# Optimization experiments

Hardware: AMD Instinct MI355X
Metric: run time of the kernel (lower is better)

## Reference

```python
import jax, jax.numpy as jnp
import numpy as np

H, SK, SV, PK, PV = 12, 16, 16, 4, 8
SCALAR_DIM, PAIR_DIM = 384, 128
SIZES = [SK*H, SK*H, SV*H, PK*H*3, PK*H*3, PV*H*3]  # qkv split sizes
N_LOGITS = 3
SS = (N_LOGITS * SK) ** -0.5                 # scalar logit scale
PS = (N_LOGITS * PK * 4.5) ** -0.5           # point logit scale
PBS = N_LOGITS ** -0.5                       # pair bias scale
EPS = 1e-8


def setup_inputs() -> dict:
    key = jax.random.key(0)
    ks = jax.random.split(key, 16)
    b, n = 1, 768
    scalar_feats = jax.random.normal(ks[0], (b, n, SCALAR_DIM), jnp.float32)
    pair_feats = jax.random.normal(ks[1], (b, n, n, PAIR_DIM), jnp.float32)
    rotations = jax.random.normal(ks[2], (b, n, 3, 3), jnp.float32)
    translations = jax.random.normal(ks[3], (b, n, 3), jnp.float32)
    mask = jnp.ones((b, n), dtype=bool)
    d_qkv = sum(SIZES)
    sc = SCALAR_DIM ** -0.5
    Wqkv = jax.random.normal(ks[4], (SCALAR_DIM, d_qkv), jnp.float32) * sc
    Wpb = jax.random.normal(ks[5], (PAIR_DIM, H), jnp.float32) * PAIR_DIM ** -0.5
    point_weights = jnp.full((1, H, 1, 1), float(np.log(np.e - 1.0)), jnp.float32)
    dim_out = H * (PAIR_DIM + SV + 4 * PV)  # 2112
    Wout = jax.random.normal(ks[6], (dim_out, SCALAR_DIM), jnp.float32) * dim_out ** -0.5
    bout = jnp.zeros((SCALAR_DIM,), jnp.float32)
    Wp1 = jax.random.normal(ks[7], (3 * H, PAIR_DIM), jnp.float32) * (3 * H) ** -0.5
    bp1 = jnp.zeros((PAIR_DIM,), jnp.float32)
    Wp2 = jax.random.normal(ks[8], (PAIR_DIM, PAIR_DIM), jnp.float32) * PAIR_DIM ** -0.5
    bp2 = jnp.zeros((PAIR_DIM,), jnp.float32)
    return dict(scalar_feats=scalar_feats, pair_feats=pair_feats, rotations=rotations,
                translations=translations, mask=mask, Wqkv=Wqkv, Wpb=Wpb,
                point_weights=point_weights, Wout=Wout, bout=bout,
                Wp1=Wp1, bp1=bp1, Wp2=Wp2, bp2=bp2)


def _heads(x, b, n, d):
    # b n (h d) -> b h n d
    return x.reshape(b, n, H, d).transpose(0, 2, 1, 3)


def _merge(x):
    # b h n d -> b n (h d)
    b, h, n, d = x.shape
    return x.transpose(0, 2, 1, 3).reshape(b, n, h * d)


def ipa_forward(scalar_feats, pair_feats, rotations, translations, mask,
                Wqkv, Wpb, point_weights, Wout, bout, Wp1, bp1, Wp2, bp2):
    b, n, _ = scalar_feats.shape
    qkv = scalar_feats @ Wqkv
    offs = np.cumsum([0] + SIZES)
    qs, ks_, vs, qp, kp, vp = [qkv[..., offs[i]:offs[i + 1]] for i in range(6)]
    qs, ks_, vs = _heads(qs, b, n, SK), _heads(ks_, b, n, SK), _heads(vs, b, n, SV)

    def to_global_points(p, d):
        p = p.reshape(b, n, H * d, 3)                       # ... (d c) -> ... d c
        p = jnp.einsum('bixy,bidy->bidx', rotations, p) + translations[:, :, None, :]
        return p.reshape(b, n, H, d, 3).transpose(0, 2, 1, 3, 4)  # b h n d 3

    qp, kp = to_global_points(qp, PK), to_global_points(kp, PK)
    vp = to_global_points(vp, PV)

    scalar_logits = jnp.einsum('bhid,bhjd->bhij', qs, ks_)
    pair_bias = jnp.einsum('bijd,dh->bhij', pair_feats, Wpb)
    point_logits = jnp.einsum('bhidc,bhjdc->bhij', qp, kp) * jax.nn.softplus(point_weights)

    m2 = mask[:, None, :, None] & mask[:, None, None, :]    # b 1 i j
    neg = -jnp.finfo(scalar_logits.dtype).max
    scalar_logits = jnp.where(m2, scalar_logits, neg)
    point_logits = jnp.where(m2, point_logits, neg)
    pair_bias = jnp.where(m2, pair_bias, neg)

    attn = jax.nn.softmax(SS * scalar_logits + PS * point_logits + PBS * pair_bias, axis=-1)

    res_scalar = jnp.einsum('bhij,bhjd->bhid', attn, vs)
    res_pair = jnp.einsum('bhij,bijd->bhid', attn, pair_feats)
    res_pts = jnp.einsum('bhij,bhjdc->bhidc', attn, vp)
    # inverse rigid: R^T (p - t)
    local = jnp.einsum('biyx,bhidy->bhidx', rotations,
                       res_pts - translations[:, None, :, None, :])
    pts_norm = jnp.sqrt(jnp.sum(local ** 2, axis=-1) + EPS)  # safe_norm

    feats = jnp.concatenate([
        _merge(res_scalar),                                   # b n h*SV
        _merge(res_pair),                                     # b n h*PAIR_DIM
        _merge(local.reshape(b, H, n, PV * 3)),               # b n h*PV*3
        _merge(pts_norm),                                     # b n h*PV
    ], axis=-1)
    scalar_out = feats @ Wout + bout

    edge = jnp.concatenate([attn,
                            jax.nn.softmax(point_logits, axis=-1),
                            jax.nn.softmax(scalar_logits, axis=-1)], axis=1)
    edge = edge.transpose(0, 2, 3, 1)                         # b i j (3h)
    pair_out = jax.nn.gelu(edge @ Wp1 + bp1, approximate=False) @ Wp2 + bp2
    return scalar_out, pair_out


def reference(scalar_feats, pair_feats, rotations, translations, mask,
              Wqkv, Wpb, point_weights, Wout, bout, Wp1, bp1, Wp2, bp2):
    return ipa_forward(scalar_feats, pair_feats, rotations, translations, mask,
                       Wqkv, Wpb, point_weights, Wout, bout, Wp1, bp1, Wp2, bp2)
```

## Files before the change

### kernel.cpp

```cpp
#include <hip/hip_runtime.h>
#include <hip/hip_bf16.h>
#include <math.h>

#define NRES 768
#define NH 12
#define DQKV 1152
#define PAIRD 128
#define SCD 384
#define DOUTF 2112

#define SS_C 0.14433756729740643f
#define PS_C 0.13608276348795434f
#define PBS_C 0.5773502691896258f

typedef __attribute__((ext_vector_type(4))) float f32x4;
typedef __attribute__((ext_vector_type(8))) short s16x8;

__device__ __forceinline__ unsigned short f2bf(float x) {
  union { float f; unsigned u; } v; v.f = x;
  unsigned r = (v.u + 0x7fffu + ((v.u >> 16) & 1u)) >> 16;
  return (unsigned short)r;
}
__device__ __forceinline__ float bf2f(unsigned short h) {
  union { unsigned u; float f; } v; v.u = (unsigned)h << 16;
  return v.f;
}

__device__ __forceinline__ float gelu_f(float x) {
  float z = x * 0.70710678118654752f;
  float az = fabsf(z);
  float t = __builtin_amdgcn_rcpf(1.f + 0.3275911f * az);
  float poly = t * (0.254829592f + t * (-0.284496736f +
               t * (1.421413741f + t * (-1.453152027f + t * 1.061405429f))));
  float e = __expf(-az * az);
  float erfv = 1.f - poly * e;
  erfv = (z < 0.f) ? -erfv : erfv;
  return 0.5f * x * (1.f + erfv);
}

__global__ __launch_bounds__(256) void gemm_bf16(
    const unsigned short* __restrict__ A, const unsigned short* __restrict__ Bt,
    const float* __restrict__ bias, float* __restrict__ C,
    int M, int Nn, int K)
{
  __shared__ __align__(16) unsigned short A_lds[64][72];
  __shared__ __align__(16) unsigned short B_lds[64][72];
  int m0 = blockIdx.y * 64, n0 = blockIdx.x * 64;
  int t = threadIdx.x;
  int lane = t & 63, w = t >> 6;
  int n15 = lane & 15, q = lane >> 4;
  f32x4 acc[4];
#pragma unroll
  for (int nt = 0; nt < 4; ++nt) acc[nt] = (f32x4){0.f, 0.f, 0.f, 0.f};
  for (int k0 = 0; k0 < K; k0 += 64) {
    __syncthreads();
#pragma unroll
    for (int u = 0; u < 2; ++u) {
      int idx = t + u * 256;
      int r = idx >> 3, c = (idx & 7) * 8;
      *(s16x8*)&A_lds[r][c] = *(const s16x8*)&A[(size_t)(m0 + r) * K + k0 + c];
      *(s16x8*)&B_lds[r][c] = *(const s16x8*)&Bt[(size_t)(n0 + r) * K + k0 + c];
    }
    __syncthreads();
#pragma unroll
    for (int ks = 0; ks < 2; ++ks) {
      s16x8 af = *(const s16x8*)&A_lds[w * 16 + n15][ks * 32 + q * 8];
#pragma unroll
      for (int nt = 0; nt < 4; ++nt) {
        s16x8 bf = *(const s16x8*)&B_lds[nt * 16 + n15][ks * 32 + q * 8];
        acc[nt] = __builtin_amdgcn_mfma_f32_16x16x32_bf16(af, bf, acc[nt], 0, 0, 0);
      }
    }
  }
#pragma unroll
  for (int nt = 0; nt < 4; ++nt) {
    int n = n0 + nt * 16 + n15;
    float bv = bias ? bias[n] : 0.f;
#pragma unroll
    for (int r = 0; r < 4; ++r) {
      int m = m0 + w * 16 + q * 4 + r;
      C[(size_t)m * Nn + n] = acc[nt][r] + bv;
    }
  }
}

__global__ __launch_bounds__(256) void prep_wqkv_kernel(
    const float* __restrict__ W, unsigned short* __restrict__ Bt)
{
  __shared__ float tile[32][33];
  int k0 = blockIdx.x * 32, n0 = blockIdx.y * 32;
  int t = threadIdx.x;
  int x = t & 31, y = t >> 5;
#pragma unroll
  for (int r = 0; r < 32; r += 8)
    tile[y + r][x] = W[(size_t)(k0 + y + r) * DQKV + n0 + x];
  __syncthreads();
#pragma unroll
  for (int r = 0; r < 32; r += 8) {
    float v = tile[x][y + r];
    unsigned short hi = f2bf(v);
    unsigned short lo = f2bf(v - bf2f(hi));
    size_t nrow = (size_t)(n0 + y + r) * 1152;
    Bt[nrow + k0 + x]       = hi;
    Bt[nrow + 384 + k0 + x] = lo;
    Bt[nrow + 768 + k0 + x] = hi;
  }
}

__global__ __launch_bounds__(128) void prep_a_kernel(
    const float* __restrict__ A, unsigned short* __restrict__ Ap)
{
  int i = blockIdx.x, t = threadIdx.x;
#pragma unroll
  for (int p = 0; p < 3; ++p) {
    int c = t + p * 128;
    float v = A[(size_t)i * SCD + c];
    unsigned short hi = f2bf(v);
    unsigned short lo = f2bf(v - bf2f(hi));
    size_t row = (size_t)i * 1152;
    Ap[row + c]       = hi;
    Ap[row + 384 + c] = hi;
    Ap[row + 768 + c] = lo;
  }
}

__global__ __launch_bounds__(256) void wt_kernel(
    const float* __restrict__ W, unsigned short* __restrict__ Wt)
{
  __shared__ float tile[32][33];
  int k0 = blockIdx.x * 32, n0 = blockIdx.y * 32;
  int t = threadIdx.x;
  int x = t & 31, y = t >> 5;
#pragma unroll
  for (int r = 0; r < 32; r += 8)
    tile[y + r][x] = W[(size_t)(k0 + y + r) * SCD + n0 + x];
  __syncthreads();
#pragma unroll
  for (int r = 0; r < 32; r += 8)
    Wt[(size_t)(n0 + y + r) * DOUTF + k0 + x] = f2bf(tile[x][y + r]);
}

__global__ __launch_bounds__(192) void points_kernel(
    const float* __restrict__ qkv, const float* __restrict__ rot,
    const float* __restrict__ trans, float* __restrict__ QP,
    float* __restrict__ KP, float* __restrict__ VP, float* __restrict__ Kq)
{
  int i = blockIdx.x;
  int t = threadIdx.x;
  const float* R = rot + (size_t)i * 9;
  const float* T = trans + (size_t)i * 3;
  int base; float* outp;
  if (t < 48) { int h = t >> 2, d = t & 3; base = 576 + (h * 4 + d) * 3;
    outp = QP + ((size_t)h * NRES + i) * 12 + d * 3; }
  else if (t < 96) { int u = t - 48; int h = u >> 2, d = u & 3; base = 720 + (h * 4 + d) * 3;
    outp = KP + ((size_t)h * NRES + i) * 12 + d * 3; }
  else { int u = t - 96; int h = u >> 3, d = u & 7; base = 864 + (h * 8 + d) * 3;
    outp = VP + ((size_t)h * NRES + i) * 24 + d * 3; }
  const float* p = qkv + (size_t)i * DQKV + base;
  float p0 = p[0], p1 = p[1], p2 = p[2];
#pragma unroll
  for (int x = 0; x < 3; ++x)
    outp[x] = R[x * 3 + 0] * p0 + R[x * 3 + 1] * p1 + R[x * 3 + 2] * p2 + T[x];
  {
    int h = t >> 4, d = t & 15;
    Kq[((size_t)h * NRES + i) * 16 + d] = qkv[(size_t)i * DQKV + 192 + h * 16 + d];
  }
}

__global__ __launch_bounds__(256) void vt_kernel(
    const float* __restrict__ qkv, const float* __restrict__ VP,
    unsigned short* __restrict__ Vt)
{
  int b = blockIdx.x;
  int h = b / 48, o = b % 48;
  int t = threadIdx.x;
  for (int p = 0; p < 3; ++p) {
    int j = p * 256 + t;
    float v;
    if (o < 16) v = qkv[(size_t)j * DQKV + 384 + h * 16 + o];
    else if (o < 40) v = VP[((size_t)h * NRES + j) * 24 + (o - 16)];
    else v = 0.f;
    Vt[((size_t)h * 48 + o) * NRES + j] = f2bf(v);
  }
}

__global__ __launch_bounds__(256) void pair_bias_kernel(
    const float* __restrict__ pair, const float* __restrict__ Wpb,
    float* __restrict__ Lb, unsigned short* __restrict__ pair_bT)
{
  __shared__ __align__(16) unsigned short Bt[64][136];
  int jt = blockIdx.x, i = blockIdx.y;
  int j0 = jt * 64;
  int t = threadIdx.x;
  int lane = t & 63, w = t >> 6;
  int n15 = lane & 15, q = lane >> 4;
  s16x8 wf[4];
#pragma unroll
  for (int ks = 0; ks < 4; ++ks) {
#pragma unroll
    for (int jj = 0; jj < 8; ++jj) {
      int k = ks * 32 + q * 8 + jj;
      float v = (n15 < 12) ? Wpb[k * 12 + n15] : 0.f;
      wf[ks][jj] = (short)f2bf(v);
    }
  }
  {
    int dq = t & 31, jb = t >> 5;
    for (int p = 0; p < 8; ++p) {
      int j = p * 8 + jb;
      float4 v = *(const float4*)(pair + ((size_t)i * NRES + j0 + j) * PAIRD + dq * 4);
      unsigned lo = (unsigned)f2bf(v.x) | ((unsigned)f2bf(v.y) << 16);
      unsigned hi = (unsigned)f2bf(v.z) | ((unsigned)f2bf(v.w) << 16);
      uint2 pk; pk.x = lo; pk.y = hi;
      *(uint2*)&Bt[j][dq * 4] = pk;
    }
  }
  __syncthreads();
  f32x4 acc = {0.f, 0.f, 0.f, 0.f};
  int m = w * 16 + n15;
#pragma unroll
  for (int ks = 0; ks < 4; ++ks) {
    s16x8 af = *(const s16x8*)&Bt[m][ks * 32 + q * 8];
    acc = __builtin_amdgcn_mfma_f32_16x16x32_bf16(af, wf[ks], acc, 0, 0, 0);
  }
  if (n15 < 12) {
    int j = j0 + w * 16 + q * 4;
    float4 st; st.x = acc[0]; st.y = acc[1]; st.z = acc[2]; st.w = acc[3];
    *(float4*)(Lb + ((size_t)n15 * NRES + i) * NRES + j) = st;
  }
  {
    int d = t >> 1, jh = t & 1;
#pragma unroll
    for (int c = 0; c < 4; ++c) {
      s16x8 pk;
#pragma unroll
      for (int e = 0; e < 8; ++e)
        pk[e] = (short)Bt[jh * 32 + c * 8 + e][d];
      *(s16x8*)&pair_bT[((size_t)i * PAIRD + d) * NRES + j0 + jh * 32 + c * 8] = pk;
    }
  }
}

#define RL 4
__global__ __launch_bounds__(256) void logits_softmax_kernel(
    const float* __restrict__ qkv, const float* __restrict__ Kq,
    const float* __restrict__ QP, const float* __restrict__ KP,
    const float* __restrict__ pw, const float* __restrict__ Lb,
    unsigned short* __restrict__ attn_b, unsigned short* __restrict__ sp_b,
    unsigned short* __restrict__ ss_b)
{
  int it = blockIdx.x, h = blockIdx.y;
  int i0 = it * RL;
  int t = threadIdx.x;
  __shared__ float q_sh[RL][28];
  if (t < RL * 28) {
    int r = t / 28, c = t % 28;
    q_sh[r][c] = (c < 16) ? qkv[(size_t)(i0 + r) * DQKV + h * 16 + c]
                          : QP[((size_t)h * NRES + i0 + r) * 12 + (c - 16)];
  }
  __syncthreads();
  float spw = log1pf(expf(pw[h]));
  float s[RL][3], p[RL][3], c[RL][3];
#pragma unroll
  for (int e = 0; e < 3; ++e) {
    int j = t + e * 256;
    float kr[16];
    const float* kq = Kq + ((size_t)h * NRES + j) * 16;
    *(float4*)&kr[0]  = *(const float4*)(kq + 0);
    *(float4*)&kr[4]  = *(const float4*)(kq + 4);
    *(float4*)&kr[8]  = *(const float4*)(kq + 8);
    *(float4*)&kr[12] = *(const float4*)(kq + 12);
    float kp[12];
    const float* kpp = KP + ((size_t)h * NRES + j) * 12;
    *(float4*)&kp[0] = *(const float4*)(kpp + 0);
    *(float4*)&kp[4] = *(const float4*)(kpp + 4);
    *(float4*)&kp[8] = *(const float4*)(kpp + 8);
#pragma unroll
    for (int r = 0; r < RL; ++r) {
      float sv = 0.f;
#pragma unroll
      for (int d = 0; d < 16; ++d) sv += q_sh[r][d] * kr[d];
      float pv = 0.f;
#pragma unroll
      for (int d = 0; d < 12; ++d) pv += q_sh[r][16 + d] * kp[d];
      pv *= spw;
      float bv = Lb[((size_t)h * NRES + i0 + r) * NRES + j];
      s[r][e] = sv; p[r][e] = pv;
      c[r][e] = SS_C * sv + PS_C * pv + PBS_C * bv;
    }
  }
  __shared__ float redm[4][RL][3];
  __shared__ float redsu[4][RL][3];
  int wv = t >> 6;
#pragma unroll
  for (int r = 0; r < RL; ++r) {
    float ms = fmaxf(fmaxf(s[r][0], s[r][1]), s[r][2]);
    float mp = fmaxf(fmaxf(p[r][0], p[r][1]), p[r][2]);
    float mc = fmaxf(fmaxf(c[r][0], c[r][1]), c[r][2]);
#pragma unroll
    for (int o = 32; o > 0; o >>= 1) {
      ms = fmaxf(ms, __shfl_down(ms, o));
      mp = fmaxf(mp, __shfl_down(mp, o));
      mc = fmaxf(mc, __shfl_down(mc, o));
    }
    if ((t & 63) == 0) { redm[wv][r][0] = ms; redm[wv][r][1] = mp; redm[wv][r][2] = mc; }
  }
  __syncthreads();
  float Ms[RL], Mp[RL], Mc[RL];
#pragma unroll
  for (int r = 0; r < RL; ++r) {
    Ms[r] = fmaxf(fmaxf(redm[0][r][0], redm[1][r][0]), fmaxf(redm[2][r][0], redm[3][r][0]));
    Mp[r] = fmaxf(fmaxf(redm[0][r][1], redm[1][r][1]), fmaxf(redm[2][r][1], redm[3][r][1]));
    Mc[r] = fmaxf(fmaxf(redm[0][r][2], redm[1][r][2]), fmaxf(redm[2][r][2], redm[3][r][2]));
  }
#pragma unroll
  for (int r = 0; r < RL; ++r) {
    float sums = 0.f, sump = 0.f, sumc = 0.f;
#pragma unroll
    for (int e = 0; e < 3; ++e) {
      float es = __expf(s[r][e] - Ms[r]); s[r][e] = es; sums += es;
      float ep = __expf(p[r][e] - Mp[r]); p[r][e] = ep; sump += ep;
      float ec = __expf(c[r][e] - Mc[r]); c[r][e] = ec; sumc += ec;
    }
#pragma unroll
    for (int o = 32; o > 0; o >>= 1) {
      sums += __shfl_down(sums, o);
      sump += __shfl_down(sump, o);
      sumc += __shfl_down(sumc, o);
    }
    if ((t & 63) == 0) { redsu[wv][r][0] = sums; redsu[wv][r][1] = sump; redsu[wv][r][2] = sumc; }
  }
  __syncthreads();
#pragma unroll
  for (int r = 0; r < RL; ++r) {
    float rs = 1.f / (redsu[0][r][0] + redsu[1][r][0] + redsu[2][r][0] + redsu[3][r][0]);
    float rp = 1.f / (redsu[0][r][1] + redsu[1][r][1] + redsu[2][r][1] + redsu[3][r][1]);
    float rc = 1.f / (redsu[0][r][2] + redsu[1][r][2] + redsu[2][r][2] + redsu[3][r][2]);
    size_t off = ((size_t)h * NRES + i0 + r) * NRES;
#pragma unroll
    for (int e = 0; e < 3; ++e) {
      int j = t + e * 256;
      ss_b[off + j]   = f2bf(s[r][e] * rs);
      sp_b[off + j]   = f2bf(p[r][e] * rp);
      attn_b[off + j] = f2bf(c[r][e] * rc);
    }
  }
}

__global__ __launch_bounds__(192) void res_sv_kernel(
    const unsigned short* __restrict__ attn, const unsigned short* __restrict__ Vt,
    float* __restrict__ res_sv)
{
  __shared__ __align__(16) unsigned short A_lds[16][72];
  __shared__ __align__(16) unsigned short B_lds[48][72];
  int it = blockIdx.x, h = blockIdx.y;
  int i0 = it * 16;
  int t = threadIdx.x;
  int lane = t & 63, w = t >> 6;
  int n15 = lane & 15, q = lane >> 4;
  f32x4 acc = {0.f, 0.f, 0.f, 0.f};
  for (int jt = 0; jt < 12; ++jt) {
    int j0 = jt * 64;
    __syncthreads();
    for (int idx = t; idx < 512; idx += 192) {
      int r = idx >> 5, j2 = idx & 31;
      *(unsigned*)&A_lds[r][j2 * 2] =
          *(const unsigned*)&attn[((size_t)h * NRES + i0 + r) * NRES + j0 + j2 * 2];
    }
    for (int idx = t; idx < 1536; idx += 192) {
      int o = idx >> 5, j2 = idx & 31;
      *(unsigned*)&B_lds[o][j2 * 2] =
          *(const unsigned*)&Vt[((size_t)h * 48 + o) * NRES + j0 + j2 * 2];
    }
    __syncthreads();
#pragma unroll
    for (int ks = 0; ks < 2; ++ks) {
      s16x8 af = *(const s16x8*)&A_lds[n15][ks * 32 + q * 8];
      s16x8 bf = *(const s16x8*)&B_lds[w * 16 + n15][ks * 32 + q * 8];
      acc = __builtin_amdgcn_mfma_f32_16x16x32_bf16(af, bf, acc, 0, 0, 0);
    }
  }
  int o = w * 16 + n15;
  if (o < 40) {
#pragma unroll
    for (int r = 0; r < 4; ++r) {
      int i = i0 + q * 4 + r;
      res_sv[((size_t)h * NRES + i) * 40 + o] = acc[r];
    }
  }
}

__global__ __launch_bounds__(256) void res_pair_kernel(
    const unsigned short* __restrict__ attn, const unsigned short* __restrict__ pair_bT,
    float* __restrict__ res_pair)
{
  __shared__ __align__(16) unsigned short A_lds[16][72];
  __shared__ __align__(16) unsigned short B_lds[128][72];
  int i = blockIdx.x;
  int t = threadIdx.x;
  int lane = t & 63, w = t >> 6;
  int n15 = lane & 15, q = lane >> 4;
  for (int idx = t; idx < 4 * 72; idx += 256)
    A_lds[12 + idx / 72][idx % 72] = 0;
  f32x4 acc[2];
  acc[0] = (f32x4){0.f, 0.f, 0.f, 0.f};
  acc[1] = (f32x4){0.f, 0.f, 0.f, 0.f};
  for (int jt = 0; jt < 12; ++jt) {
    int j0 = jt * 64;
    __syncthreads();
    for (int idx = t; idx < 384; idx += 256) {
      int r = idx >> 5, j2 = idx & 31;
      *(unsigned*)&A_lds[r][j2 * 2] =
          *(const unsigned*)&attn[((size_t)r * NRES + i) * NRES + j0 + j2 * 2];
    }
#pragma unroll
    for (int p = 0; p < 4; ++p) {
      int chunk = t + p * 256;
      int d = chunk >> 3, jc = (chunk & 7) * 8;
      *(s16x8*)&B_lds[d][jc] =
          *(const s16x8*)&pair_bT[((size_t)i * PAIRD + d) * NRES + j0 + jc];
    }
    __syncthreads();
#pragma unroll
    for (int ks = 0; ks < 2; ++ks) {
      s16x8 af = *(const s16x8*)&A_lds[n15][ks * 32 + q * 8];
#pragma unroll
      for (int nt = 0; nt < 2; ++nt) {
        int o = (w * 2 + nt) * 16 + n15;
        s16x8 bf = *(const s16x8*)&B_lds[o][ks * 32 + q * 8];
        acc[nt] = __builtin_amdgcn_mfma_f32_16x16x32_bf16(af, bf, acc[nt], 0, 0, 0);
      }
    }
  }
#pragma unroll
  for (int nt = 0; nt < 2; ++nt) {
    int o = (w * 2 + nt) * 16 + n15;
#pragma unroll
    for (int r = 0; r < 4; ++r) {
      int hh = q * 4 + r;
      if (hh < 12)
        res_pair[((size_t)hh * NRES + i) * PAIRD + o] = acc[nt][r];
    }
  }
}

__global__ __launch_bounds__(256) void feats_kernel(
    const float* __restrict__ res_sv, const float* __restrict__ res_pair,
    const float* __restrict__ rot, const float* __restrict__ trans,
    unsigned short* __restrict__ feats)
{
  int i = blockIdx.x;
  int t = threadIdx.x;
  unsigned short* F = feats + (size_t)i * DOUTF;
  if (t < 192) {
    int h = t >> 4, d = t & 15;
    F[t] = f2bf(res_sv[((size_t)h * NRES + i) * 40 + d]);
  }
  for (int e = 0; e < 6; ++e) {
    int idx = e * 256 + t;
    int h = idx >> 7, o = idx & 127;
    F[192 + idx] = f2bf(res_pair[((size_t)h * NRES + i) * PAIRD + o]);
  }
  if (t < 96) {
    int h = t >> 3, d = t & 7;
    const float* R = rot + (size_t)i * 9;
    const float* T = trans + (size_t)i * 3;
    const float* pp = res_sv + ((size_t)h * NRES + i) * 40 + 16 + d * 3;
    float p0 = pp[0] - T[0], p1 = pp[1] - T[1], p2 = pp[2] - T[2];
    float l0 = R[0] * p0 + R[3] * p1 + R[6] * p2;
    float l1 = R[1] * p0 + R[4] * p1 + R[7] * p2;
    float l2 = R[2] * p0 + R[5] * p1 + R[8] * p2;
    F[1728 + h * 24 + d * 3 + 0] = f2bf(l0);
    F[1728 + h * 24 + d * 3 + 1] = f2bf(l1);
    F[1728 + h * 24 + d * 3 + 2] = f2bf(l2);
    F[2016 + h * 8 + d] = f2bf(sqrtf(l0 * l0 + l1 * l1 + l2 * l2 + 1e-8f));
  }
}

__global__ __launch_bounds__(256) void mlp_kernel(
    const unsigned short* __restrict__ attn, const unsigned short* __restrict__ sp,
    const unsigned short* __restrict__ ss, const float* __restrict__ Wp1,
    const float* __restrict__ bp1, const float* __restrict__ Wp2,
    const float* __restrict__ bp2, float* __restrict__ out)
{
  __shared__ __align__(16) unsigned short E_lds[2][64][72];
  __shared__ __align__(16) unsigned short A_lds[2][64][136];
  int t = threadIdx.x;
  int lane = t & 63, w = t >> 6;
  int n15 = lane & 15, q = lane >> 4;
  for (int idx = t; idx < 64 * 28 * 2; idx += 256) {
    int b = idx / (64 * 28);
    int r = (idx / 28) % 64, k = 36 + idx % 28;
    E_lds[b][r][k] = 0;
  }
  s16x8 w1f[2][2], w2f[4][2];
#pragma unroll
  for (int ks = 0; ks < 2; ++ks)
#pragma unroll
    for (int nt = 0; nt < 2; ++nt) {
      int nn = (w * 2 + nt) * 16 + n15;
#pragma unroll
      for (int jj = 0; jj < 8; ++jj) {
        int k = ks * 32 + q * 8 + jj;
        w1f[ks][nt][jj] = (k < 36) ? (short)f2bf(Wp1[(size_t)k * 128 + nn]) : (short)0;
      }
    }
#pragma unroll
  for (int ks = 0; ks < 4; ++ks)
#pragma unroll
    for (int nt = 0; nt < 2; ++nt) {
      int nn = (w * 2 + nt) * 16 + n15;
#pragma unroll
      for (int jj = 0; jj < 8; ++jj) {
        int k = ks * 32 + q * 8 + jj;
        w2f[ks][nt][jj] = (short)f2bf(Wp2[(size_t)k * 128 + nn]);
      }
    }
  float b1v[2], b2v[2];
#pragma unroll
  for (int nt = 0; nt < 2; ++nt) {
    int nn = (w * 2 + nt) * 16 + n15;
    b1v[nt] = bp1[nn];
    b2v[nt] = bp2[nn];
  }
  const unsigned short* bufs[3] = {attn, sp, ss};
  const int NT = NRES * 12;
  int ej = t & 63, ecb = t >> 6;
  int tile = blockIdx.x;
  int cur = 0;
  int prevTile = -1;
  if (tile < NT) {
    int i = tile / 12, j0 = (tile % 12) * 64;
#pragma unroll
    for (int p = 0; p < 9; ++p) {
      int cc = ecb * 9 + p;
      E_lds[0][ej][cc] = bufs[cc / 12][((size_t)(cc % 12) * NRES + i) * NRES + j0 + ej];
    }
  }
  __syncthreads();
  for (; tile < NT; tile += gridDim.x) {
    int nxt = tile + gridDim.x;
    unsigned short ev[9];
    if (nxt < NT) {
      int i2 = nxt / 12, j02 = (nxt % 12) * 64;
#pragma unroll
      for (int p = 0; p < 9; ++p) {
        int cc = ecb * 9 + p;
        ev[p] = bufs[cc / 12][((size_t)(cc % 12) * NRES + i2) * NRES + j02 + ej];
      }
    }
    f32x4 c1[4][2];
#pragma unroll
    for (int mt = 0; mt < 4; ++mt) {
#pragma unroll
      for (int nt = 0; nt < 2; ++nt) c1[mt][nt] = (f32x4){0.f, 0.f, 0.f, 0.f};
#pragma unroll
      for (int ks = 0; ks < 2; ++ks) {
        s16x8 af = *(const s16x8*)&E_lds[cur][mt * 16 + n15][ks * 32 + q * 8];
#pragma unroll
        for (int nt = 0; nt < 2; ++nt)
          c1[mt][nt] = __builtin_amdgcn_mfma_f32_16x16x32_bf16(af, w1f[ks][nt], c1[mt][nt], 0, 0, 0);
      }
    }
    if (prevTile >= 0) {
      f32x4 c2[4][2];
#pragma unroll
      for (int mt = 0; mt < 4; ++mt) {
#pragma unroll
        for (int nt = 0; nt < 2; ++nt) c2[mt][nt] = (f32x4){0.f, 0.f, 0.f, 0.f};
#pragma unroll
        for (int ks = 0; ks < 4; ++ks) {
          s16x8 af = *(const s16x8*)&A_lds[cur ^ 1][mt * 16 + n15][ks * 32 + q * 8];
#pragma unroll
          for (int nt = 0; nt < 2; ++nt)
            c2[mt][nt] = __builtin_amdgcn_mfma_f32_16x16x32_bf16(af, w2f[ks][nt], c2[mt][nt], 0, 0, 0);
        }
      }
      int ip = prevTile / 12, j0p = (prevTile % 12) * 64;
#pragma unroll
      for (int mt = 0; mt < 4; ++mt)
#pragma unroll
        for (int nt = 0; nt < 2; ++nt) {
          int o = (w * 2 + nt) * 16 + n15;
          int jb = j0p + mt * 16 + q * 4;
#pragma unroll
          for (int r = 0; r < 4; ++r)
            out[((size_t)ip * NRES + jb + r) * PAIRD + o] = c2[mt][nt][r] + b2v[nt];
        }
    }
#pragma unroll
    for (int mt = 0; mt < 4; ++mt)
#pragma unroll
      for (int nt = 0; nt < 2; ++nt) {
        int o = (w * 2 + nt) * 16 + n15;
#pragma unroll
        for (int r = 0; r < 4; ++r) {
          float x = c1[mt][nt][r] + b1v[nt];
          A_lds[cur][mt * 16 + q * 4 + r][o] = f2bf(gelu_f(x));
        }
      }
    if (nxt < NT) {
#pragma unroll
      for (int p = 0; p < 9; ++p)
        E_lds[cur ^ 1][ej][ecb * 9 + p] = ev[p];
    }
    __syncthreads();
    prevTile = tile;
    cur ^= 1;
  }
  if (prevTile >= 0) {
    f32x4 c2[4][2];
#pragma unroll
    for (int mt = 0; mt < 4; ++mt) {
#pragma unroll
      for (int nt = 0; nt < 2; ++nt) c2[mt][nt] = (f32x4){0.f, 0.f, 0.f, 0.f};
#pragma unroll
      for (int ks = 0; ks < 4; ++ks) {
        s16x8 af = *(const s16x8*)&A_lds[cur ^ 1][mt * 16 + n15][ks * 32 + q * 8];
#pragma unroll
        for (int nt = 0; nt < 2; ++nt)
          c2[mt][nt] = __builtin_amdgcn_mfma_f32_16x16x32_bf16(af, w2f[ks][nt], c2[mt][nt], 0, 0, 0);
      }
    }
    int ip = prevTile / 12, j0p = (prevTile % 12) * 64;
#pragma unroll
    for (int mt = 0; mt < 4; ++mt)
#pragma unroll
      for (int nt = 0; nt < 2; ++nt) {
        int o = (w * 2 + nt) * 16 + n15;
        int jb = j0p + mt * 16 + q * 4;
#pragma unroll
        for (int r = 0; r < 4; ++r)
          out[((size_t)ip * NRES + jb + r) * PAIRD + o] = c2[mt][nt][r] + b2v[nt];
      }
  }
}

extern "C" void kernel_launch(void* const* d_in, const int* in_sizes, int n_in,
                              void* d_out, int out_size, void* d_ws, size_t ws_size,
                              hipStream_t stream) {
  const float* scalar_feats = (const float*)d_in[0];
  const float* pair  = (const float*)d_in[1];
  const float* rot   = (const float*)d_in[2];
  const float* trans = (const float*)d_in[3];
  const float* Wqkv  = (const float*)d_in[5];
  const float* Wpb   = (const float*)d_in[6];
  const float* pw    = (const float*)d_in[7];
  const float* Wout  = (const float*)d_in[8];
  const float* bout  = (const float*)d_in[9];
  const float* Wp1   = (const float*)d_in[10];
  const float* bp1   = (const float*)d_in[11];
  const float* Wp2   = (const float*)d_in[12];
  const float* bp2   = (const float*)d_in[13];
  float* out = (float*)d_out;
  float* ws = (float*)d_ws;

  float* qkv = ws;
  float* QP  = ws + 884736;
  float* KP  = ws + 995328;
  float* VP  = ws + 1105920;
  unsigned short* Vt = (unsigned short*)(ws + 1327104);
  float* Lb  = ws + 1548288;
  unsigned short* attn_b = (unsigned short*)(ws + 8626176);
  unsigned short* sp_b   = (unsigned short*)(ws + 12165120);
  unsigned short* ss_b   = (unsigned short*)(ws + 15704064);
  float* res_sv   = ws + 19243008;
  float* res_pair = ws + 19611648;
  unsigned short* feats_b = (unsigned short*)(ws + 20791296);
  unsigned short* Wout_t  = (unsigned short*)(ws + 21602304);
  float* Kq = ws + 22007808;
  unsigned short* Aprime  = (unsigned short*)(ws + 22155264);
  unsigned short* Wqkv_t  = (unsigned short*)(ws + 22597632);
  unsigned short* pair_bT = (unsigned short*)(ws + 23261184);

  prep_wqkv_kernel<<<dim3(SCD / 32, DQKV / 32), 256, 0, stream>>>(Wqkv, Wqkv_t);
  prep_a_kernel<<<NRES, 128, 0, stream>>>(scalar_feats, Aprime);
  gemm_bf16<<<dim3(DQKV / 64, NRES / 64), 256, 0, stream>>>(
      Aprime, Wqkv_t, nullptr, qkv, NRES, DQKV, 1152);
  points_kernel<<<NRES, 192, 0, stream>>>(qkv, rot, trans, QP, KP, VP, Kq);
  vt_kernel<<<576, 256, 0, stream>>>(qkv, VP, Vt);
  pair_bias_kernel<<<dim3(12, NRES), 256, 0, stream>>>(pair, Wpb, Lb, pair_bT);
  logits_softmax_kernel<<<dim3(NRES / RL, 12), 256, 0, stream>>>(
      qkv, Kq, QP, KP, pw, Lb, attn_b, sp_b, ss_b);
  res_sv_kernel<<<dim3(48, 12), 192, 0, stream>>>(attn_b, Vt, res_sv);
  res_pair_kernel<<<NRES, 256, 0, stream>>>(attn_b, pair_bT, res_pair);
  feats_kernel<<<NRES, 256, 0, stream>>>(res_sv, res_pair, rot, trans, feats_b);
  wt_kernel<<<dim3(DOUTF / 32, SCD / 32), 256, 0, stream>>>(Wout, Wout_t);
  gemm_bf16<<<dim3(SCD / 64, NRES / 64), 256, 0, stream>>>(
      feats_b, Wout_t, bout, out, NRES, SCD, DOUTF);
  mlp_kernel<<<2304, 256, 0, stream>>>(attn_b, sp_b, ss_b, Wp1, bp1, Wp2, bp2, out + 294912);
}
```

Baseline: 867.9 us.

## Fuse pair result into feats, retile res_sv, rework pair_bT transpose store

The res_pair kernel now writes bf16 results straight into the feats buffer, so the fp32 res_pair intermediate and its copy pass in feats_kernel go away. res_sv_kernel is retiled to 64 rows per block with 16-byte vector loads and three accumulators per wave, cutting the number of blocks and reloads of Vt. The pair_bT transpose in pair_bias_kernel is remapped so each thread writes one contiguous 8-element chunk, reading LDS in a rotated order to avoid bank conflicts. The retiled res_sv launches only 144 blocks, which may underfill the GPU.

```diff
diff --git a/kernel.cpp b/kernel.cpp
--- a/kernel.cpp
+++ b/kernel.cpp
@@ -229,14 +229,17 @@
     *(float4*)(Lb + ((size_t)n15 * NRES + i) * NRES + j) = st;
   }
   {
-    int d = t >> 1, jh = t & 1;
-#pragma unroll
-    for (int c = 0; c < 4; ++c) {
+    int d8 = t >> 3, js = t & 7;
+#pragma unroll
+    for (int p = 0; p < 4; ++p) {
+      int d = p * 32 + d8;
       s16x8 pk;
 #pragma unroll
-      for (int e = 0; e < 8; ++e)
-        pk[e] = (short)Bt[jh * 32 + c * 8 + e][d];
-      *(s16x8*)&pair_bT[((size_t)i * PAIRD + d) * NRES + j0 + jh * 32 + c * 8] = pk;
+      for (int e = 0; e < 8; ++e) {
+        int ee = (e + js) & 7;
+        pk[ee] = (short)Bt[js * 8 + ee][d];
+      }
+      *(s16x8*)&pair_bT[((size_t)i * PAIRD + d) * NRES + j0 + js * 8] = pk;
     }
   }
 }
@@ -347,52 +350,64 @@
   }
 }
 
-__global__ __launch_bounds__(192) void res_sv_kernel(
+__global__ __launch_bounds__(256) void res_sv_kernel(
     const unsigned short* __restrict__ attn, const unsigned short* __restrict__ Vt,
     float* __restrict__ res_sv)
 {
-  __shared__ __align__(16) unsigned short A_lds[16][72];
+  __shared__ __align__(16) unsigned short A_lds[64][72];
   __shared__ __align__(16) unsigned short B_lds[48][72];
   int it = blockIdx.x, h = blockIdx.y;
-  int i0 = it * 16;
+  int i0 = it * 64;
   int t = threadIdx.x;
   int lane = t & 63, w = t >> 6;
   int n15 = lane & 15, q = lane >> 4;
-  f32x4 acc = {0.f, 0.f, 0.f, 0.f};
+  f32x4 acc[3];
+  acc[0] = acc[1] = acc[2] = (f32x4){0.f, 0.f, 0.f, 0.f};
   for (int jt = 0; jt < 12; ++jt) {
     int j0 = jt * 64;
     __syncthreads();
-    for (int idx = t; idx < 512; idx += 192) {
-      int r = idx >> 5, j2 = idx & 31;
-      *(unsigned*)&A_lds[r][j2 * 2] =
-          *(const unsigned*)&attn[((size_t)h * NRES + i0 + r) * NRES + j0 + j2 * 2];
-    }
-    for (int idx = t; idx < 1536; idx += 192) {
-      int o = idx >> 5, j2 = idx & 31;
-      *(unsigned*)&B_lds[o][j2 * 2] =
-          *(const unsigned*)&Vt[((size_t)h * 48 + o) * NRES + j0 + j2 * 2];
+#pragma unroll
+    for (int u = 0; u < 2; ++u) {
+      int idx = t + u * 256;
+      int r = idx >> 3, c = (idx & 7) * 8;
+      *(s16x8*)&A_lds[r][c] =
+          *(const s16x8*)&attn[((size_t)h * NRES + i0 + r) * NRES + j0 + c];
+    }
+    {
+      int r = t >> 3, c = (t & 7) * 8;
+      *(s16x8*)&B_lds[r][c] = *(const s16x8*)&Vt[((size_t)h * 48 + r) * NRES + j0 + c];
+      if (t < 128) {
+        int r2 = 32 + (t >> 3);
+        *(s16x8*)&B_lds[r2][c] = *(const s16x8*)&Vt[((size_t)h * 48 + r2) * NRES + j0 + c];
+      }
     }
     __syncthreads();
 #pragma unroll
     for (int ks = 0; ks < 2; ++ks) {
-      s16x8 af = *(const s16x8*)&A_lds[n15][ks * 32 + q * 8];
-      s16x8 bf = *(const s16x8*)&B_lds[w * 16 + n15][ks * 32 + q * 8];
-      acc = __builtin_amdgcn_mfma_f32_16x16x32_bf16(af, bf, acc, 0, 0, 0);
-    }
-  }
-  int o = w * 16 + n15;
-  if (o < 40) {
-#pragma unroll
-    for (int r = 0; r < 4; ++r) {
-      int i = i0 + q * 4 + r;
-      res_sv[((size_t)h * NRES + i) * 40 + o] = acc[r];
+      s16x8 af = *(const s16x8*)&A_lds[w * 16 + n15][ks * 32 + q * 8];
+#pragma unroll
+      for (int nt = 0; nt < 3; ++nt) {
+        s16x8 bf = *(const s16x8*)&B_lds[nt * 16 + n15][ks * 32 + q * 8];
+        acc[nt] = __builtin_amdgcn_mfma_f32_16x16x32_bf16(af, bf, acc[nt], 0, 0, 0);
+      }
+    }
+  }
+#pragma unroll
+  for (int nt = 0; nt < 3; ++nt) {
+    int o = nt * 16 + n15;
+    if (o < 40) {
+#pragma unroll
+      for (int r = 0; r < 4; ++r) {
+        int i = i0 + w * 16 + q * 4 + r;
+        res_sv[((size_t)h * NRES + i) * 40 + o] = acc[nt][r];
+      }
     }
   }
 }
 
 __global__ __launch_bounds__(256) void res_pair_kernel(
     const unsigned short* __restrict__ attn, const unsigned short* __restrict__ pair_bT,
-    float* __restrict__ res_pair)
+    unsigned short* __restrict__ feats_b)
 {
   __shared__ __align__(16) unsigned short A_lds[16][72];
   __shared__ __align__(16) unsigned short B_lds[128][72];
@@ -439,27 +454,21 @@
     for (int r = 0; r < 4; ++r) {
       int hh = q * 4 + r;
       if (hh < 12)
-        res_pair[((size_t)hh * NRES + i) * PAIRD + o] = acc[nt][r];
-    }
-  }
-}
-
-__global__ __launch_bounds__(256) void feats_kernel(
-    const float* __restrict__ res_sv, const float* __restrict__ res_pair,
-    const float* __restrict__ rot, const float* __restrict__ trans,
-    unsigned short* __restrict__ feats)
+        feats_b[(size_t)i * DOUTF + 192 + hh * PAIRD + o] = f2bf(acc[nt][r]);
+    }
+  }
+}
+
+__global__ __launch_bounds__(192) void feats_kernel(
+    const float* __restrict__ res_sv, const float* __restrict__ rot,
+    const float* __restrict__ trans, unsigned short* __restrict__ feats)
 {
   int i = blockIdx.x;
   int t = threadIdx.x;
   unsigned short* F = feats + (size_t)i * DOUTF;
-  if (t < 192) {
+  {
     int h = t >> 4, d = t & 15;
     F[t] = f2bf(res_sv[((size_t)h * NRES + i) * 40 + d]);
-  }
-  for (int e = 0; e < 6; ++e) {
-    int idx = e * 256 + t;
-    int h = idx >> 7, o = idx & 127;
-    F[192 + idx] = f2bf(res_pair[((size_t)h * NRES + i) * PAIRD + o]);
   }
   if (t < 96) {
     int h = t >> 3, d = t & 7;
@@ -665,7 +674,6 @@
   unsigned short* sp_b   = (unsigned short*)(ws + 12165120);
   unsigned short* ss_b   = (unsigned short*)(ws + 15704064);
   float* res_sv   = ws + 19243008;
-  float* res_pair = ws + 19611648;
   unsigned short* feats_b = (unsigned short*)(ws + 20791296);
   unsigned short* Wout_t  = (unsigned short*)(ws + 21602304);
   float* Kq = ws + 22007808;
@@ -682,9 +690,9 @@
   pair_bias_kernel<<<dim3(12, NRES), 256, 0, stream>>>(pair, Wpb, Lb, pair_bT);
   logits_softmax_kernel<<<dim3(NRES / RL, 12), 256, 0, stream>>>(
       qkv, Kq, QP, KP, pw, Lb, attn_b, sp_b, ss_b);
-  res_sv_kernel<<<dim3(48, 12), 192, 0, stream>>>(attn_b, Vt, res_sv);
-  res_pair_kernel<<<NRES, 256, 0, stream>>>(attn_b, pair_bT, res_pair);
-  feats_kernel<<<NRES, 256, 0, stream>>>(res_sv, res_pair, rot, trans, feats_b);
+  res_sv_kernel<<<dim3(12, 12), 256, 0, stream>>>(attn_b, Vt, res_sv);
+  res_pair_kernel<<<NRES, 256, 0, stream>>>(attn_b, pair_bT, feats_b);
+  feats_kernel<<<NRES, 192, 0, stream>>>(res_sv, rot, trans, feats_b);
   wt_kernel<<<dim3(DOUTF / 32, SCD / 32), 256, 0, stream>>>(Wout, Wout_t);
   gemm_bf16<<<dim3(SCD / 64, NRES / 64), 256, 0, stream>>>(
       feats_b, Wout_t, bout, out, NRES, SCD, DOUTF);
```

After: 828.3 us. -4.6%, faster.
